# Optimization experiments

Hardware: AMD Instinct MI355X
Metric: run time of the kernel (lower is better)

The kernel has to match this reference:

```python
import jax, jax.numpy as jnp
import numpy as np

EOS = 1e-10
N_NODES = 100000
N_EDGES = 1600000
IN_DIM = 256
HID = 64
ALPHA = 0.1
TEMP = 1.0
BIAS = 1e-4


def setup_inputs() -> dict:
    key = jax.random.key(0)
    k1, k2, k3, k4, k5 = jax.random.split(key, 5)
    features = jax.random.normal(k1, (N_NODES, IN_DIM), dtype=jnp.float32)
    edges = jax.random.randint(k2, (2, N_EDGES), 0, N_NODES, dtype=jnp.int64)
    noise = jax.random.uniform(k3, (N_EDGES,), dtype=jnp.float32)
    # params: embedding Linear(input_dim, hidden) and edge_mlp Linear(2*hidden, 1)
    W_emb = jax.random.normal(k4, (IN_DIM, HID), dtype=jnp.float32) / np.sqrt(IN_DIM)
    b_emb = jnp.zeros((HID,), dtype=jnp.float32)
    W_edge = jax.random.normal(k5, (2 * HID,), dtype=jnp.float32) / np.sqrt(2 * HID)
    b_edge = jnp.zeros((), dtype=jnp.float32)
    return {"features": features, "edges": edges, "noise": noise,
            "W_emb": W_emb, "b_emb": b_emb, "W_edge": W_edge, "b_edge": b_edge}


def _edge_weight_norm_both(src, dst, w, n_nodes):
    # DGL EdgeWeightNorm(norm='both'): w_e / sqrt(outdeg_w(src) * indeg_w(dst))
    deg_out = jax.ops.segment_sum(w, src, num_segments=n_nodes)
    deg_in = jax.ops.segment_sum(w, dst, num_segments=n_nodes)
    return w / jnp.sqrt(deg_out[src] * deg_in[dst])


def reference(features, edges, noise, W_emb, b_emb, W_edge, b_edge):
    src, dst = edges[0], edges[1]
    E = src.shape[0]
    # node embedding: relu(Linear(features))
    h = jax.nn.relu(features @ W_emb + b_emb)  # [N, H]
    # edge score: edge_mlp(cat(h[u], h[v])) symmetrized.
    # split W_edge -> score = h[u]@W1 + h[v]@W2 + b  (avoids materializing concat)
    p1 = h @ W_edge[:HID]   # [N]
    p2 = h @ W_edge[HID:]   # [N]
    s1 = p1[src] + p2[dst] + b_edge
    s2 = p1[dst] + p2[src] + b_edge
    raw = (s1 + s2) * 0.5   # [E]
    # gumbel sigmoid sampling
    eps = (BIAS - (1.0 - BIAS)) * noise + (1.0 - BIAS)
    gate = jnp.log(eps) - jnp.log1p(-eps)
    weights_lp = jax.nn.sigmoid((gate + raw) / TEMP)  # [E]
    weights_hp = 1.0 - weights_lp
    # weight_to_adj: add self loops with weight 1, then EdgeWeightNorm 'both'
    loop = jnp.arange(N_NODES, dtype=src.dtype)
    src_f = jnp.concatenate([src, loop])
    dst_f = jnp.concatenate([dst, loop])
    ones_n = jnp.ones((N_NODES,), dtype=weights_lp.dtype)
    w_lp_full = jnp.concatenate([weights_lp, ones_n]) + EOS
    w_lp_norm = _edge_weight_norm_both(src_f, dst_f, w_lp_full, N_NODES)
    w_hp_full = jnp.concatenate([weights_hp, ones_n]) + EOS
    w_hp_norm = _edge_weight_norm_both(src_f, dst_f, w_hp_full, N_NODES)
    w_hp_norm = w_hp_norm * (-ALPHA)
    w_hp_norm = w_hp_norm.at[E:].set(1.0)  # self-loop weights forced to 1
    return (w_lp_norm, w_hp_norm, weights_lp, weights_hp)
```

## Files before the change

kernel.cpp:

```cpp
#include <hip/hip_runtime.h>
#include <hip/hip_bf16.h>
#include <math.h>

#define N_NODESC 100000
#define N_EDGESC 1600000
#define IN_DIMC 256
#define HIDC 64
#define ALPHAC 0.1f
#define BIASC 1e-4f
#define EOSC 1e-10f

#define MC (N_EDGESC + N_NODESC)
#define NBUCK 400
#define NBUCK_USED 391
#define BSHIFT 8
#define BMASK 255
#define BCAP 5120u
#define W20SCALE 1048576.0f
#define W20INV (1.0f / 1048576.0f)
#define SUMMASK ((1ull << 40) - 1)
#define CNTONE (1ull << 40)
#define EPB 4
#define NWAVE 8

typedef __attribute__((ext_vector_type(8))) short short8;
typedef __attribute__((ext_vector_type(4))) float f32x4;

#define WT_STRIDE 264

__device__ inline void load_edge(const int* __restrict__ edges, int e, int is64,
                                 int& src, int& dst) {
    if (is64) {
        const int2 a = ((const int2*)edges)[e];
        const int2 b = ((const int2*)edges)[N_EDGESC + e];
        src = a.x; dst = b.x;
    } else {
        src = edges[e];
        dst = edges[N_EDGESC + e];
    }
}

__device__ inline short pkbf(float x) {
    union { __hip_bfloat16 b; short s; } u;
    u.b = __float2bfloat16(x);
    return u.s;
}

__global__ __launch_bounds__(256, 3) void node_kernel(
    const float* __restrict__ features,
    const float* __restrict__ W_emb,
    const float* __restrict__ b_emb,
    const float* __restrict__ W_edge,
    const int* __restrict__ edges,
    float* __restrict__ q,
    unsigned long long* __restrict__ cursor64,
    int* __restrict__ flag) {
    __shared__ __align__(16) short Wt[HIDC * WT_STRIDE];
    const int tid = threadIdx.x;
    if (blockIdx.x == 0) {
        if (tid == 0) {
            int z = 0;
            #pragma unroll
            for (int i = 0; i < 16; ++i) z |= edges[2 * i + 1];
            *flag = (z == 0) ? 1 : 0;
        }
        for (int b = tid; b < NBUCK; b += 256) cursor64[b] = 0ull;
    }
    {
        const float4* Wg = (const float4*)W_emb;
        #pragma unroll
        for (int i = 0; i < 16; ++i) {
            const int f4 = tid + 256 * i;
            const float4 g = Wg[f4];
            const int flat = 4 * f4;
            const int k = flat >> 6;
            const int j0 = flat & 63;
            Wt[(j0 + 0) * WT_STRIDE + k] = pkbf(g.x);
            Wt[(j0 + 1) * WT_STRIDE + k] = pkbf(g.y);
            Wt[(j0 + 2) * WT_STRIDE + k] = pkbf(g.z);
            Wt[(j0 + 3) * WT_STRIDE + k] = pkbf(g.w);
        }
    }
    const int lane = tid & 63;
    const int wave = tid >> 6;
    const int quad = lane >> 4;
    const int m = lane & 15;
    f32x4 accA[4], accB[4];
    float wsum4[4];
    #pragma unroll
    for (int nt = 0; nt < 4; ++nt) {
        const int j = m + 16 * nt;
        const float b = b_emb[j];
        accA[nt] = (f32x4){b, b, b, b};
        accB[nt] = (f32x4){b, b, b, b};
        wsum4[nt] = W_edge[j] + W_edge[HIDC + j];
    }
    __syncthreads();

    const int node0A = blockIdx.x * 128 + wave * 16;
    const int node0B = node0A + 64;
    const float* frA = features + (size_t)min(node0A + m, N_NODESC - 1) * IN_DIMC;
    const float* frB = features + (size_t)min(node0B + m, N_NODESC - 1) * IN_DIMC;

    #pragma unroll
    for (int ks = 0; ks < 8; ++ks) {
        const int kk = ks * 32 + quad * 8;
        const float4 fa0 = *(const float4*)(frA + kk);
        const float4 fb0 = *(const float4*)(frA + kk + 4);
        const float4 fa1 = *(const float4*)(frB + kk);
        const float4 fb1 = *(const float4*)(frB + kk + 4);
        short8 afA, afB;
        afA[0] = pkbf(fa0.x); afA[1] = pkbf(fa0.y);
        afA[2] = pkbf(fa0.z); afA[3] = pkbf(fa0.w);
        afA[4] = pkbf(fb0.x); afA[5] = pkbf(fb0.y);
        afA[6] = pkbf(fb0.z); afA[7] = pkbf(fb0.w);
        afB[0] = pkbf(fa1.x); afB[1] = pkbf(fa1.y);
        afB[2] = pkbf(fa1.z); afB[3] = pkbf(fa1.w);
        afB[4] = pkbf(fb1.x); afB[5] = pkbf(fb1.y);
        afB[6] = pkbf(fb1.z); afB[7] = pkbf(fb1.w);
        #pragma unroll
        for (int nt = 0; nt < 4; ++nt) {
            const short8 bf =
                *(const short8*)&Wt[(m + 16 * nt) * WT_STRIDE + kk];
            accA[nt] = __builtin_amdgcn_mfma_f32_16x16x32_bf16(afA, bf, accA[nt],
                                                               0, 0, 0);
            accB[nt] = __builtin_amdgcn_mfma_f32_16x16x32_bf16(afB, bf, accB[nt],
                                                               0, 0, 0);
        }
    }

    #pragma unroll
    for (int r = 0; r < 4; ++r) {
        float sA = 0.f, sB = 0.f;
        #pragma unroll
        for (int nt = 0; nt < 4; ++nt) {
            sA = fmaf(fmaxf(accA[nt][r], 0.f), wsum4[nt], sA);
            sB = fmaf(fmaxf(accB[nt][r], 0.f), wsum4[nt], sB);
        }
        sA += __shfl_xor(sA, 1); sA += __shfl_xor(sA, 2);
        sA += __shfl_xor(sA, 4); sA += __shfl_xor(sA, 8);
        sB += __shfl_xor(sB, 1); sB += __shfl_xor(sB, 2);
        sB += __shfl_xor(sB, 4); sB += __shfl_xor(sB, 8);
        if (m == 0) {
            const int nA = node0A + quad * 4 + r;
            const int nB = node0B + quad * 4 + r;
            if (nA < N_NODESC) q[nA] = sA;
            if (nB < N_NODESC) q[nB] = sB;
        }
    }
}

__global__ __launch_bounds__(512) void edge_scatter(
    const int* __restrict__ edges,
    const float* __restrict__ noise,
    const float* __restrict__ b_edge,
    const float* __restrict__ q,
    unsigned long long* __restrict__ cursor64,
    unsigned* __restrict__ recS,
    unsigned* __restrict__ recD,
    float* __restrict__ out,
    const int* __restrict__ flag) {
    __shared__ unsigned hist[2][NWAVE][NBUCK];
    __shared__ unsigned wbase[2][NWAVE][NBUCK];
    const int tid = threadIdx.x;
    const int wave = tid >> 6;
    for (int i = tid; i < 2 * NWAVE * NBUCK; i += 512)
        ((unsigned*)hist)[i] = 0u;
    __syncthreads();
    const int is64 = *flag;
    const float be = b_edge[0];
    const int e0 = blockIdx.x * (512 * EPB) + tid;

    int sA[EPB], dA[EPB];
    #pragma unroll
    for (int i = 0; i < EPB; ++i) {
        const int e = e0 + i * 512;
        sA[i] = -1;
        if (e < N_EDGESC) load_edge(edges, e, is64, sA[i], dA[i]);
    }
    float qs[EPB], qd[EPB];
    #pragma unroll
    for (int i = 0; i < EPB; ++i) {
        if (sA[i] >= 0) { qs[i] = q[sA[i]]; qd[i] = q[dA[i]]; }
    }
    float wlpA[EPB];
    unsigned rkS[EPB], rkD[EPB];
    #pragma unroll
    for (int i = 0; i < EPB; ++i) {
        if (sA[i] >= 0) {
            const int e = e0 + i * 512;
            const float raw = 0.5f * (qs[i] + qd[i]) + be;
            const float u = noise[e];
            const float eps = (BIASC - (1.0f - BIASC)) * u + (1.0f - BIASC);
            const float gate = logf(eps) - log1pf(-eps);
            const float wlp = 1.0f / (1.0f + expf(-(gate + raw)));
            wlpA[i] = wlp;
            out[2 * MC + e] = wlp;
            out[2 * MC + N_EDGESC + e] = 1.0f - wlp;
            rkS[i] = atomicAdd(&hist[0][wave][sA[i] >> BSHIFT], 1u);
            rkD[i] = atomicAdd(&hist[1][wave][dA[i] >> BSHIFT], 1u);
        }
    }
    __syncthreads();
    if (tid < NBUCK) {
        const int b = tid;
        unsigned ps[NWAVE], pd[NWAVE];
        unsigned totS = 0, totD = 0;
        #pragma unroll
        for (int w = 0; w < NWAVE; ++w) {
            ps[w] = totS; totS += hist[0][w][b];
            pd[w] = totD; totD += hist[1][w][b];
        }
        const unsigned long long add =
            (unsigned long long)totS | ((unsigned long long)totD << 32);
        const unsigned long long old = atomicAdd(&cursor64[b], add);
        const unsigned baseS = (unsigned)old;
        const unsigned baseD = (unsigned)(old >> 32);
        #pragma unroll
        for (int w = 0; w < NWAVE; ++w) {
            wbase[0][w][b] = baseS + ps[w];
            wbase[1][w][b] = baseD + pd[w];
        }
    }
    __syncthreads();
    #pragma unroll
    for (int i = 0; i < EPB; ++i) {
        if (sA[i] >= 0) {
            const int s = sA[i], d = dA[i];
            const unsigned w20 =
                min((unsigned)(wlpA[i] * W20SCALE + 0.5f), 0xFFFFFu);
            const unsigned pS = wbase[0][wave][s >> BSHIFT] + rkS[i];
            const unsigned pD = wbase[1][wave][d >> BSHIFT] + rkD[i];
            if (pS < BCAP)
                recS[(unsigned)(s >> BSHIFT) * BCAP + pS] =
                    ((unsigned)(s & BMASK) << 20) | w20;
            if (pD < BCAP)
                recD[(unsigned)(d >> BSHIFT) * BCAP + pD] =
                    ((unsigned)(d & BMASK) << 20) | w20;
        }
    }
}

__global__ __launch_bounds__(256) void gather_kernel(
    const unsigned* __restrict__ recS,
    const unsigned* __restrict__ recD,
    const unsigned long long* __restrict__ cursor64,
    float2* __restrict__ rS,
    float2* __restrict__ rD,
    float* __restrict__ out) {
    __shared__ unsigned long long table[512];
    const int bkt = blockIdx.x;
    const unsigned long long c = cursor64[bkt];
    const unsigned cntS = min((unsigned)c, BCAP);
    const unsigned cntD = min((unsigned)(c >> 32), BCAP);
    const unsigned* rs = recS + (unsigned)bkt * BCAP;
    const unsigned* rd = recD + (unsigned)bkt * BCAP;
    const int tid = threadIdx.x;
    table[tid] = 0ull;
    table[tid + 256] = 0ull;
    __syncthreads();
    for (unsigned i = tid; i < cntS; i += 256) {
        const unsigned r = rs[i];
        atomicAdd(&table[r >> 20], CNTONE | (unsigned long long)(r & 0xFFFFFu));
    }
    for (unsigned i = tid; i < cntD; i += 256) {
        const unsigned r = rd[i];
        atomicAdd(&table[256 + (r >> 20)],
                  CNTONE | (unsigned long long)(r & 0xFFFFFu));
    }
    __syncthreads();
    const int node = (bkt << BSHIFT) + tid;
    if (node < N_NODESC) {
        const unsigned long long aS = table[tid];
        const unsigned long long aD = table[tid + 256];
        const float sumS = (float)(aS & SUMMASK) * W20INV;
        const float cS = (float)(aS >> 40);
        const float sumD = (float)(aD & SUMMASK) * W20INV;
        const float cD = (float)(aD >> 40);
        float2 vS, vD;
        vS.x = rsqrtf(1.0f + sumS);
        vS.y = rsqrtf(1.0f + cS - sumS);
        vD.x = rsqrtf(1.0f + sumD);
        vD.y = rsqrtf(1.0f + cD - sumD);
        rS[node] = vS;
        rD[node] = vD;
        out[N_EDGESC + node] = (1.0f + EOSC) * vS.x * vD.x;
        out[MC + N_EDGESC + node] = 1.0f;
    }
}

__global__ __launch_bounds__(256) void final_kernel(
    const int* __restrict__ edges,
    const float2* __restrict__ rS,
    const float2* __restrict__ rD,
    float* __restrict__ out,
    const int* __restrict__ flag) {
    const int tid = threadIdx.x;
    const int i0 = blockIdx.x * 1024 + tid;
    const int is64 = *flag;
    int sA[4], dA[4];
    float wl[4], wh[4];
    #pragma unroll
    for (int j = 0; j < 4; ++j) {
        const int i = i0 + j * 256;
        sA[j] = -1;
        if (i < N_EDGESC) load_edge(edges, i, is64, sA[j], dA[j]);
    }
    #pragma unroll
    for (int j = 0; j < 4; ++j) {
        const int i = i0 + j * 256;
        if (sA[j] >= 0) {
            const float wlp = out[2 * MC + i];
            wl[j] = wlp + EOSC;
            wh[j] = (1.0f - wlp) + EOSC;
        }
    }
    float2 a[4], b[4];
    #pragma unroll
    for (int j = 0; j < 4; ++j) {
        if (sA[j] >= 0) { a[j] = rS[sA[j]]; b[j] = rD[dA[j]]; }
    }
    #pragma unroll
    for (int j = 0; j < 4; ++j) {
        const int i = i0 + j * 256;
        if (sA[j] >= 0) {
            out[i] = wl[j] * a[j].x * b[j].x;
            out[MC + i] = -ALPHAC * wh[j] * a[j].y * b[j].y;
        }
    }
}

extern "C" void kernel_launch(void* const* d_in, const int* in_sizes, int n_in,
                              void* d_out, int out_size, void* d_ws, size_t ws_size,
                              hipStream_t stream) {
    const float* features = (const float*)d_in[0];
    const int* edges      = (const int*)d_in[1];
    const float* noise    = (const float*)d_in[2];
    const float* W_emb    = (const float*)d_in[3];
    const float* b_emb    = (const float*)d_in[4];
    const float* W_edge   = (const float*)d_in[5];
    const float* b_edge   = (const float*)d_in[6];
    float* out = (float*)d_out;
    char* ws = (char*)d_ws;

    float* q = (float*)ws;
    float2* rS = (float2*)(ws + 400000);
    float2* rD = (float2*)(ws + 1200000);
    int* flag = (int*)(ws + 2000000);
    unsigned long long* cursor64 = (unsigned long long*)(ws + 2000064);
    unsigned* recS = (unsigned*)(ws + 2097152);
    unsigned* recD = (unsigned*)(ws + 10289152);

    node_kernel<<<782, 256, 0, stream>>>(features, W_emb, b_emb, W_edge, edges,
                                         q, cursor64, flag);
    edge_scatter<<<(N_EDGESC + 512 * EPB - 1) / (512 * EPB), 512, 0, stream>>>(
        edges, noise, b_edge, q, cursor64, recS, recD, out, flag);
    gather_kernel<<<NBUCK_USED, 256, 0, stream>>>(recS, recD, cursor64, rS, rD,
                                                  out);
    final_kernel<<<(N_EDGESC + 1023) / 1024, 256, 0, stream>>>(edges, rS, rD,
                                                               out, flag);
}
```

Baseline: 263.1 us.

## Split gather into per-direction blocks and vectorize final edge kernel

The gather kernel now launches one block per bucket and direction, so the src and dst histograms are built by separate blocks. This doubles the block count for a 391-block launch that underfills the GPU. Writing the self-loop outputs moves from gather into the final kernel, which now handles four consecutive edges per thread with int4/float4 vector loads and stores. The cost is a slightly more complex tail path for the node segment and alignment assumptions on the edge and output buffers.

```diff
diff --git a/kernel.cpp b/kernel.cpp
--- a/kernel.cpp
+++ b/kernel.cpp
@@ -246,86 +246,101 @@
     const unsigned* __restrict__ recD,
     const unsigned long long* __restrict__ cursor64,
     float2* __restrict__ rS,
-    float2* __restrict__ rD,
-    float* __restrict__ out) {
-    __shared__ unsigned long long table[512];
-    const int bkt = blockIdx.x;
+    float2* __restrict__ rD) {
+    __shared__ unsigned long long table[256];
+    const int bid = blockIdx.x;
+    const int isD = bid >= NBUCK_USED;
+    const int bkt = isD ? bid - NBUCK_USED : bid;
     const unsigned long long c = cursor64[bkt];
-    const unsigned cntS = min((unsigned)c, BCAP);
-    const unsigned cntD = min((unsigned)(c >> 32), BCAP);
-    const unsigned* rs = recS + (unsigned)bkt * BCAP;
-    const unsigned* rd = recD + (unsigned)bkt * BCAP;
+    const unsigned cnt = min((unsigned)(isD ? (c >> 32) : c), BCAP);
+    const unsigned* rec = (isD ? recD : recS) + (unsigned)bkt * BCAP;
     const int tid = threadIdx.x;
     table[tid] = 0ull;
-    table[tid + 256] = 0ull;
-    __syncthreads();
-    for (unsigned i = tid; i < cntS; i += 256) {
-        const unsigned r = rs[i];
+    __syncthreads();
+    for (unsigned i = tid; i < cnt; i += 256) {
+        const unsigned r = rec[i];
         atomicAdd(&table[r >> 20], CNTONE | (unsigned long long)(r & 0xFFFFFu));
-    }
-    for (unsigned i = tid; i < cntD; i += 256) {
-        const unsigned r = rd[i];
-        atomicAdd(&table[256 + (r >> 20)],
-                  CNTONE | (unsigned long long)(r & 0xFFFFFu));
     }
     __syncthreads();
     const int node = (bkt << BSHIFT) + tid;
     if (node < N_NODESC) {
-        const unsigned long long aS = table[tid];
-        const unsigned long long aD = table[tid + 256];
-        const float sumS = (float)(aS & SUMMASK) * W20INV;
-        const float cS = (float)(aS >> 40);
-        const float sumD = (float)(aD & SUMMASK) * W20INV;
-        const float cD = (float)(aD >> 40);
-        float2 vS, vD;
-        vS.x = rsqrtf(1.0f + sumS);
-        vS.y = rsqrtf(1.0f + cS - sumS);
-        vD.x = rsqrtf(1.0f + sumD);
-        vD.y = rsqrtf(1.0f + cD - sumD);
-        rS[node] = vS;
-        rD[node] = vD;
-        out[N_EDGESC + node] = (1.0f + EOSC) * vS.x * vD.x;
-        out[MC + N_EDGESC + node] = 1.0f;
-    }
-}
-
-__global__ __launch_bounds__(256) void final_kernel(
+        const unsigned long long a = table[tid];
+        const float sum = (float)(a & SUMMASK) * W20INV;
+        const float cf = (float)(a >> 40);
+        float2 r;
+        r.x = rsqrtf(1.0f + sum);
+        r.y = rsqrtf(1.0f + cf - sum);
+        (isD ? rD : rS)[node] = r;
+    }
+}
+
+__global__ __launch_bounds__(512) void final_kernel(
     const int* __restrict__ edges,
     const float2* __restrict__ rS,
     const float2* __restrict__ rD,
     float* __restrict__ out,
     const int* __restrict__ flag) {
-    const int tid = threadIdx.x;
-    const int i0 = blockIdx.x * 1024 + tid;
-    const int is64 = *flag;
-    int sA[4], dA[4];
-    float wl[4], wh[4];
-    #pragma unroll
-    for (int j = 0; j < 4; ++j) {
-        const int i = i0 + j * 256;
-        sA[j] = -1;
-        if (i < N_EDGESC) load_edge(edges, i, is64, sA[j], dA[j]);
-    }
-    #pragma unroll
-    for (int j = 0; j < 4; ++j) {
-        const int i = i0 + j * 256;
-        if (sA[j] >= 0) {
-            const float wlp = out[2 * MC + i];
-            wl[j] = wlp + EOSC;
-            wh[j] = (1.0f - wlp) + EOSC;
-        }
-    }
-    float2 a[4], b[4];
-    #pragma unroll
-    for (int j = 0; j < 4; ++j) {
-        if (sA[j] >= 0) { a[j] = rS[sA[j]]; b[j] = rD[dA[j]]; }
-    }
-    #pragma unroll
-    for (int j = 0; j < 4; ++j) {
-        const int i = i0 + j * 256;
-        if (sA[j] >= 0) {
-            out[i] = wl[j] * a[j].x * b[j].x;
-            out[MC + i] = -ALPHAC * wh[j] * a[j].y * b[j].y;
+    const int i0 = (blockIdx.x * 512 + threadIdx.x) * 4;
+    if (i0 >= MC) return;
+    if (i0 + 4 <= N_EDGESC) {
+        const int is64 = *flag;
+        int s[4], d[4];
+        if (is64) {
+            const int4 a0 = ((const int4*)edges)[i0 >> 1];
+            const int4 a1 = ((const int4*)edges)[(i0 >> 1) + 1];
+            const int4 b0 = ((const int4*)edges)[(N_EDGESC + i0) >> 1];
+            const int4 b1 = ((const int4*)edges)[((N_EDGESC + i0) >> 1) + 1];
+            s[0] = a0.x; s[1] = a0.z; s[2] = a1.x; s[3] = a1.z;
+            d[0] = b0.x; d[1] = b0.z; d[2] = b1.x; d[3] = b1.z;
+        } else {
+            const int4 a = ((const int4*)edges)[i0 >> 2];
+            const int4 b = ((const int4*)edges)[(N_EDGESC + i0) >> 2];
+            s[0] = a.x; s[1] = a.y; s[2] = a.z; s[3] = a.w;
+            d[0] = b.x; d[1] = b.y; d[2] = b.z; d[3] = b.w;
+        }
+        const float4 w4 = *(const float4*)&out[2 * MC + i0];
+        float2 av[4], bv[4];
+        #pragma unroll
+        for (int j = 0; j < 4; ++j) { av[j] = rS[s[j]]; bv[j] = rD[d[j]]; }
+        const float wl[4] = {w4.x + EOSC, w4.y + EOSC, w4.z + EOSC, w4.w + EOSC};
+        const float wh[4] = {(1.0f - w4.x) + EOSC, (1.0f - w4.y) + EOSC,
+                             (1.0f - w4.z) + EOSC, (1.0f - w4.w) + EOSC};
+        float4 o1, o2;
+        o1.x = wl[0] * av[0].x * bv[0].x;
+        o1.y = wl[1] * av[1].x * bv[1].x;
+        o1.z = wl[2] * av[2].x * bv[2].x;
+        o1.w = wl[3] * av[3].x * bv[3].x;
+        o2.x = -ALPHAC * wh[0] * av[0].y * bv[0].y;
+        o2.y = -ALPHAC * wh[1] * av[1].y * bv[1].y;
+        o2.z = -ALPHAC * wh[2] * av[2].y * bv[2].y;
+        o2.w = -ALPHAC * wh[3] * av[3].y * bv[3].y;
+        *(float4*)&out[i0] = o1;
+        *(float4*)&out[MC + i0] = o2;
+    } else {
+        const int n0 = i0 - N_EDGESC;
+        float4 o1;
+        float* o1p = (float*)&o1;
+        #pragma unroll
+        for (int j = 0; j < 4; ++j) {
+            const int n = n0 + j;
+            o1p[j] = 0.f;
+            if (n < N_NODESC) {
+                const float2 a = rS[n];
+                const float2 b = rD[n];
+                o1p[j] = (1.0f + EOSC) * a.x * b.x;
+            }
+        }
+        if (n0 + 4 <= N_NODESC) {
+            *(float4*)&out[i0] = o1;
+            *(float4*)&out[MC + i0] = (float4){1.f, 1.f, 1.f, 1.f};
+        } else {
+            #pragma unroll
+            for (int j = 0; j < 4; ++j) {
+                if (n0 + j < N_NODESC) {
+                    out[i0 + j] = o1p[j];
+                    out[MC + i0 + j] = 1.0f;
+                }
+            }
         }
     }
 }
@@ -355,8 +370,8 @@
                                          q, cursor64, flag);
     edge_scatter<<<(N_EDGESC + 512 * EPB - 1) / (512 * EPB), 512, 0, stream>>>(
         edges, noise, b_edge, q, cursor64, recS, recD, out, flag);
-    gather_kernel<<<NBUCK_USED, 256, 0, stream>>>(recS, recD, cursor64, rS, rD,
-                                                  out);
-    final_kernel<<<(N_EDGESC + 1023) / 1024, 256, 0, stream>>>(edges, rS, rD,
-                                                               out, flag);
-}
+    gather_kernel<<<2 * NBUCK_USED, 256, 0, stream>>>(recS, recD, cursor64, rS,
+                                                      rD);
+    final_kernel<<<(MC / 4 + 511) / 512, 512, 0, stream>>>(edges, rS, rD, out,
+                                                           flag);
+}
```

Result: no change. 259.8 us (-1.3%).
